# Optimization experiments

Measured on AMD Instinct MI355X. Metric: run time of the kernel, lower is better.

## Reference

```python
import jax, jax.numpy as jnp
import numpy as np

B, N, K, D, H = 8, 128, 64, 256, 8  # batch, groups, keys-per-query, k_dim (=h_size), n_head


def setup_inputs() -> dict:
    key = jax.random.key(0)
    kq, kk, kv, kw, kb = jax.random.split(key, 5)
    bound = 1.0 / np.sqrt(D)  # torch nn.Bilinear default init bound
    return {
        "q": jax.random.normal(kq, (B, N, 1, D), jnp.float32),
        "k": jax.random.normal(kk, (B, N, K, D), jnp.float32),
        "v": jax.random.normal(kv, (B, N, K, D), jnp.float32),
        "W": jax.random.uniform(kw, (H, D, D), jnp.float32, -bound, bound),
        "b": jax.random.uniform(kb, (H,), jnp.float32, -bound, bound),
    }


def reference(q, k, v, W, b):
    Bs, Ns, Ks, Ds = k.shape
    Hh = W.shape[0]
    qe = q[:, :, 0, :]  # (B,N,D); torch expands q over K, einsum broadcasts instead
    # nn.Bilinear: scores[b,n,k,h] = q[b,n,:] @ W[h] @ k[b,n,k,:] + b[h]
    scores = jnp.einsum('bnd,hde,bnke->bnkh', qe, W, k) + b  # (B,N,K,H)
    # Faithful to torch's .view(B, N, -1, K): row-major reinterpretation of the
    # trailing (K, H) pair as (H, K) — a dim-mixing reshape, not a transpose.
    attn = scores.reshape(Bs, Ns, Hh, Ks)
    attn = jax.nn.softmax(attn, axis=-1)  # softmax over last dim (dropout p=0)
    # matmul(attn, v) -> (B,N,H,Dv); then sum over the head axis
    output = jnp.einsum('bnhk,bnkd->bnd', attn, v)
    return output, attn
```

## Files before the change

kernel.cpp:

```cpp
#include <hip/hip_runtime.h>
#include <math.h>

namespace {

constexpr int D = 256;
constexpr int H = 8;

typedef __attribute__((ext_vector_type(8))) short bf16x8;
typedef __attribute__((ext_vector_type(4))) float f32x4;

__device__ inline unsigned short bf16rn(float x) {
  unsigned u = __builtin_bit_cast(unsigned, x);
  u += 0x7fffu + ((u >> 16) & 1u);
  return (unsigned short)(u >> 16);
}
__device__ inline float bf16tof(unsigned short b) {
  return __builtin_bit_cast(float, (unsigned)b << 16);
}

constexpr size_t OFF_QW  = 0;
constexpr size_t OFF_WFH = (size_t)8 << 20;
constexpr size_t OFF_WFL = (size_t)9 << 20;
constexpr size_t OFF_QFH = (size_t)10 << 20;
constexpr size_t OFF_QFL = ((size_t)10 << 20) + ((size_t)512 << 10);

__global__ __launch_bounds__(256) void prep_kernel(
    const float* __restrict__ q, const float* __restrict__ W,
    char* __restrict__ ws) {
  const int gid = blockIdx.x * 256 + threadIdx.x;
  float e[8];
  char *hi_base, *lo_base;
  size_t outoff;
  if (gid < 65536) {
    const int l = gid & 63, ks = (gid >> 6) & 7, he = gid >> 9;
    const int h = he >> 4, et = he & 15;
    const int d0 = ks * 32 + ((l >> 4) << 3);
    const int ecol = et * 16 + (l & 15);
    const float* src = W + (size_t)h * 65536 + (size_t)d0 * 256 + ecol;
    #pragma unroll
    for (int j = 0; j < 8; ++j) e[j] = src[j * 256];
    hi_base = ws + OFF_WFH; lo_base = ws + OFF_WFL;
    outoff = (size_t)gid * 16;
  } else {
    const int t = gid - 65536;
    const int l = t & 63, ks = (t >> 6) & 7, bt = t >> 9;
    const int row = bt * 16 + (l & 15);
    const int d0 = ks * 32 + ((l >> 4) << 3);
    const float4* src = reinterpret_cast<const float4*>(q + (size_t)row * 256 + d0);
    float4 a = src[0], b = src[1];
    e[0] = a.x; e[1] = a.y; e[2] = a.z; e[3] = a.w;
    e[4] = b.x; e[5] = b.y; e[6] = b.z; e[7] = b.w;
    hi_base = ws + OFF_QFH; lo_base = ws + OFF_QFL;
    outoff = (size_t)t * 16;
  }
  unsigned hw[4], lw[4];
  #pragma unroll
  for (int p = 0; p < 4; ++p) {
    unsigned short h0 = bf16rn(e[2 * p]), h1 = bf16rn(e[2 * p + 1]);
    unsigned short l0 = bf16rn(e[2 * p] - bf16tof(h0));
    unsigned short l1 = bf16rn(e[2 * p + 1] - bf16tof(h1));
    hw[p] = (unsigned)h0 | ((unsigned)h1 << 16);
    lw[p] = (unsigned)l0 | ((unsigned)l1 << 16);
  }
  *reinterpret_cast<uint4*>(hi_base + outoff) = make_uint4(hw[0], hw[1], hw[2], hw[3]);
  *reinterpret_cast<uint4*>(lo_base + outoff) = make_uint4(lw[0], lw[1], lw[2], lw[3]);
}

__global__ __launch_bounds__(256) void qw_mfma_kernel(
    const char* __restrict__ ws_in, float* __restrict__ qW) {
  const int tid = threadIdx.x;
  const int w   = blockIdx.x * 4 + (tid >> 6);
  const int l   = tid & 63;
  const int bng = w >> 5;
  const int heg = w & 31;
  const char* qfh = ws_in + OFF_QFH;
  const char* qfl = ws_in + OFF_QFL;
  const char* wfh = ws_in + OFF_WFH;
  const char* wfl = ws_in + OFF_WFL;

  f32x4 acc[2][4];
  #pragma unroll
  for (int i = 0; i < 2; ++i)
    #pragma unroll
    for (int j = 0; j < 4; ++j) acc[i][j] = {0.f, 0.f, 0.f, 0.f};

  #pragma unroll 2
  for (int ks = 0; ks < 8; ++ks) {
    bf16x8 aH[2], aL[2], bH[4], bL[4];
    #pragma unroll
    for (int i = 0; i < 2; ++i) {
      const size_t off = ((size_t)((bng * 2 + i) * 8 + ks) * 64 + l) * 16;
      aH[i] = *reinterpret_cast<const bf16x8*>(qfh + off);
      aL[i] = *reinterpret_cast<const bf16x8*>(qfl + off);
    }
    #pragma unroll
    for (int j = 0; j < 4; ++j) {
      const size_t off = ((size_t)((heg * 4 + j) * 8 + ks) * 64 + l) * 16;
      bH[j] = *reinterpret_cast<const bf16x8*>(wfh + off);
      bL[j] = *reinterpret_cast<const bf16x8*>(wfl + off);
    }
    #pragma unroll
    for (int i = 0; i < 2; ++i)
      #pragma unroll
      for (int j = 0; j < 4; ++j) {
        acc[i][j] = __builtin_amdgcn_mfma_f32_16x16x32_bf16(aH[i], bH[j], acc[i][j], 0, 0, 0);
        acc[i][j] = __builtin_amdgcn_mfma_f32_16x16x32_bf16(aH[i], bL[j], acc[i][j], 0, 0, 0);
        acc[i][j] = __builtin_amdgcn_mfma_f32_16x16x32_bf16(aL[i], bH[j], acc[i][j], 0, 0, 0);
      }
  }

  const int rbase = (l >> 4) * 4;
  const int col   = l & 15;
  #pragma unroll
  for (int i = 0; i < 2; ++i)
    #pragma unroll
    for (int j = 0; j < 4; ++j) {
      const size_t cidx = (size_t)(heg * 4 + j) * 16 + col;
      #pragma unroll
      for (int r = 0; r < 4; ++r) {
        const int bn = (bng * 2 + i) * 16 + rbase + r;
        qW[(size_t)bn * 2048 + cidx] = acc[i][j][r];
      }
    }
}

constexpr int FB2   = 0;
constexpr int WSP2  = 8320;
constexpr int SMEM3 = 9344;

__global__ __launch_bounds__(256, 2) void attn_fused_kernel(
    const float* __restrict__ qW, const float* __restrict__ kin,
    const float* __restrict__ vin, const float* __restrict__ bin,
    float* __restrict__ out, float* __restrict__ attn_out) {
  __shared__ alignas(16) long long smem_ll[SMEM3 / 8];
  char* sm = reinterpret_cast<char*>(smem_ll);
  float* wsp = reinterpret_cast<float*>(sm + WSP2);
  const int tid = threadIdx.x;
  const int bn  = blockIdx.x;
  const int wid = tid >> 6;
  const int ln  = tid & 63;

  const float* arow = kin + (size_t)bn * 16384 +
                      (size_t)(wid * 16 + (ln & 15)) * 256 + ((ln >> 4) << 3);
  float4 ka[16];
  #pragma unroll
  for (int ks = 0; ks < 8; ++ks) {
    ka[2 * ks]     = *reinterpret_cast<const float4*>(arow + ks * 32);
    ka[2 * ks + 1] = *reinterpret_cast<const float4*>(arow + ks * 32 + 4);
  }
  __builtin_amdgcn_sched_barrier(0);

  const float4* qw4 = reinterpret_cast<const float4*>(qW) + (size_t)bn * 512;
  float4 qv0 = qw4[tid];
  float4 qv1 = qw4[tid + 256];
  __builtin_amdgcn_sched_barrier(0);

  const float4* v4 = reinterpret_cast<const float4*>(vin) + (size_t)bn * 4096;
  float4 vv[16];
  #pragma unroll
  for (int i = 0; i < 16; ++i) vv[i] = v4[(size_t)(wid + 4 * i) * 64 + ln];
  __builtin_amdgcn_sched_barrier(0);

  {
    const int ks = tid >> 5, slot = 32 + (tid & 31);
    *reinterpret_cast<uint4*>(sm + FB2 + ks * 1040 + slot * 16) =
        make_uint4(0u, 0u, 0u, 0u);
  }
  #pragma unroll
  for (int i = 0; i < 2; ++i) {
    int p = tid + 256 * i;
    int hh = p >> 6, equad = p & 63;
    int ks = equad >> 3, g = (equad >> 1) & 3, j0 = (equad & 1) * 4;
    int base = FB2 + ks * 1040 + (hh * 4 + g) * 16 + j0 * 2;
    float4 qv = i == 0 ? qv0 : qv1;
    unsigned short h0 = bf16rn(qv.x), h1 = bf16rn(qv.y),
                   h2 = bf16rn(qv.z), h3 = bf16rn(qv.w);
    *reinterpret_cast<uint2*>(sm + base) =
        make_uint2((unsigned)h0 | ((unsigned)h1 << 16),
                   (unsigned)h2 | ((unsigned)h3 << 16));
  }
  __syncthreads();

  const int slot_r = (ln & 15) * 4 + (ln >> 4);
  const char* pbH = sm + FB2 + slot_r * 16;
  f32x4 acc = {0.f, 0.f, 0.f, 0.f};
  #pragma unroll
  for (int ks = 0; ks < 8; ++ks) {
    const float4 a0 = ka[2 * ks], a1 = ka[2 * ks + 1];
    bf16x8 aH;
    aH[0] = (short)bf16rn(a0.x); aH[1] = (short)bf16rn(a0.y);
    aH[2] = (short)bf16rn(a0.z); aH[3] = (short)bf16rn(a0.w);
    aH[4] = (short)bf16rn(a1.x); aH[5] = (short)bf16rn(a1.y);
    aH[6] = (short)bf16rn(a1.z); aH[7] = (short)bf16rn(a1.w);
    bf16x8 bH = *reinterpret_cast<const bf16x8*>(pbH + ks * 1040);
    acc = __builtin_amdgcn_mfma_f32_16x16x32_bf16(aH, bH, acc, 0, 0, 0);
  }

  const float bias = bin[ln & 7];
  const int col = ln & 15;
  const bool valid = col < 8;
  float x0 = acc[0] + bias, x1 = acc[1] + bias, x2 = acc[2] + bias, x3 = acc[3] + bias;
  float m = valid ? fmaxf(fmaxf(x0, x1), fmaxf(x2, x3)) : -1e30f;
  m = fmaxf(m, __shfl_xor(m, 1, 64));
  m = fmaxf(m, __shfl_xor(m, 2, 64));
  m = fmaxf(m, __shfl_xor(m, 4, 64));
  m = fmaxf(m, __shfl_xor(m, 16, 64));
  float e0 = valid ? expf(x0 - m) : 0.f;
  float e1 = valid ? expf(x1 - m) : 0.f;
  float e2 = valid ? expf(x2 - m) : 0.f;
  float e3 = valid ? expf(x3 - m) : 0.f;
  float s = e0 + e1 + e2 + e3;
  s += __shfl_xor(s, 1, 64);
  s += __shfl_xor(s, 2, 64);
  s += __shfl_xor(s, 4, 64);
  s += __shfl_xor(s, 16, 64);
  float inv = 1.f / s;
  float p0 = e0 * inv, p1 = e1 * inv, p2 = e2 * inv, p3 = e3 * inv;
  if (valid) {
    size_t base = (size_t)bn * 512 + (size_t)(wid * 16 + (ln >> 4) * 4) * 8 + col;
    attn_out[base]      = p0;
    attn_out[base + 8]  = p1;
    attn_out[base + 16] = p2;
    attn_out[base + 24] = p3;
  }
  p0 += __shfl_xor(p0, 32, 64);
  p1 += __shfl_xor(p1, 32, 64);
  p2 += __shfl_xor(p2, 32, 64);
  p3 += __shfl_xor(p3, 32, 64);
  if (ln < 32 && (ln & 15) < 8) {
    const int rb = (ln >> 4) * 4;
    const int c8 = ln & 7;
    float* w = wsp + wid * 64;
    w[(rb + 0) * 8 + c8] = p0;
    w[(rb + 1) * 8 + c8] = p1;
    w[(rb + 2) * 8 + c8] = p2;
    w[(rb + 3) * 8 + c8] = p3;
  }
  __syncthreads();

  float4 av = make_float4(0.f, 0.f, 0.f, 0.f);
  #pragma unroll
  for (int i = 0; i < 16; ++i) {
    const int r = wid + 4 * i;
    float w = wsp[r] + wsp[64 + r] + wsp[128 + r] + wsp[192 + r];
    av.x += w * vv[i].x; av.y += w * vv[i].y;
    av.z += w * vv[i].z; av.w += w * vv[i].w;
  }
  float* s_red = reinterpret_cast<float*>(sm);
  *reinterpret_cast<float4*>(&s_red[wid * 260 + (ln << 2)]) = av;
  __syncthreads();

  out[(size_t)bn * D + tid] =
      s_red[tid] + s_red[260 + tid] + s_red[520 + tid] + s_red[780 + tid];
}

}

extern "C" void kernel_launch(void* const* d_in, const int* in_sizes, int n_in,
                              void* d_out, int out_size, void* d_ws, size_t ws_size,
                              hipStream_t stream) {
  const float* q = (const float*)d_in[0];
  const float* k = (const float*)d_in[1];
  const float* v = (const float*)d_in[2];
  const float* W = (const float*)d_in[3];
  const float* b = (const float*)d_in[4];

  float* out  = (float*)d_out;
  float* attn = out + 262144;
  char*  ws   = (char*)d_ws;
  float* qWbuf = (float*)(ws + OFF_QW);

  hipLaunchKernelGGL(prep_kernel,       dim3(384),  dim3(256), 0, stream, q, W, ws);
  hipLaunchKernelGGL(qw_mfma_kernel,    dim3(256),  dim3(256), 0, stream, ws, qWbuf);
  hipLaunchKernelGGL(attn_fused_kernel, dim3(1024), dim3(256), 0, stream,
                     qWbuf, k, v, b, out, attn);
}
```

Before: 44.21 us.

## Split attention block into separate score and value-accumulate warp groups

Doubles the block to 512 threads. Waves 0-3 now load k and compute the bilinear scores and softmax, while waves 4-7 load v and do the weighted sum, so each wave holds only one 16-element register array instead of two. This is meant to lower per-wave register pressure and raise memory-level parallelism and occupancy. The cost is half the threads idling in each phase and more waves per block competing for the CU.

```diff
diff --git a/kernel.cpp b/kernel.cpp
--- a/kernel.cpp
+++ b/kernel.cpp
@@ -128,7 +128,7 @@
 constexpr int WSP2  = 8320;
 constexpr int SMEM3 = 9344;
 
-__global__ __launch_bounds__(256, 2) void attn_fused_kernel(
+__global__ __launch_bounds__(512, 8) void attn_fused_kernel(
     const float* __restrict__ qW, const float* __restrict__ kin,
     const float* __restrict__ vin, const float* __restrict__ bin,
     float* __restrict__ out, float* __restrict__ attn_out) {
@@ -139,40 +139,37 @@
   const int bn  = blockIdx.x;
   const int wid = tid >> 6;
   const int ln  = tid & 63;
-
-  const float* arow = kin + (size_t)bn * 16384 +
-                      (size_t)(wid * 16 + (ln & 15)) * 256 + ((ln >> 4) << 3);
+  const bool is_score = wid < 4;
+
   float4 ka[16];
-  #pragma unroll
-  for (int ks = 0; ks < 8; ++ks) {
-    ka[2 * ks]     = *reinterpret_cast<const float4*>(arow + ks * 32);
-    ka[2 * ks + 1] = *reinterpret_cast<const float4*>(arow + ks * 32 + 4);
-  }
-  __builtin_amdgcn_sched_barrier(0);
+  float4 vv[16];
+  if (is_score) {
+    const float* arow = kin + (size_t)bn * 16384 +
+                        (size_t)(wid * 16 + (ln & 15)) * 256 + ((ln >> 4) << 3);
+    #pragma unroll
+    for (int ks = 0; ks < 8; ++ks) {
+      ka[2 * ks]     = *reinterpret_cast<const float4*>(arow + ks * 32);
+      ka[2 * ks + 1] = *reinterpret_cast<const float4*>(arow + ks * 32 + 4);
+    }
+  } else {
+    const float4* v4 = reinterpret_cast<const float4*>(vin) + (size_t)bn * 4096;
+    #pragma unroll
+    for (int i = 0; i < 16; ++i)
+      vv[i] = v4[(size_t)((wid - 4) + 4 * i) * 64 + ln];
+  }
 
   const float4* qw4 = reinterpret_cast<const float4*>(qW) + (size_t)bn * 512;
-  float4 qv0 = qw4[tid];
-  float4 qv1 = qw4[tid + 256];
-  __builtin_amdgcn_sched_barrier(0);
-
-  const float4* v4 = reinterpret_cast<const float4*>(vin) + (size_t)bn * 4096;
-  float4 vv[16];
-  #pragma unroll
-  for (int i = 0; i < 16; ++i) vv[i] = v4[(size_t)(wid + 4 * i) * 64 + ln];
-  __builtin_amdgcn_sched_barrier(0);
-
-  {
+  float4 qv = qw4[tid];
+
+  if (tid < 256) {
     const int ks = tid >> 5, slot = 32 + (tid & 31);
     *reinterpret_cast<uint4*>(sm + FB2 + ks * 1040 + slot * 16) =
         make_uint4(0u, 0u, 0u, 0u);
   }
-  #pragma unroll
-  for (int i = 0; i < 2; ++i) {
-    int p = tid + 256 * i;
-    int hh = p >> 6, equad = p & 63;
-    int ks = equad >> 3, g = (equad >> 1) & 3, j0 = (equad & 1) * 4;
-    int base = FB2 + ks * 1040 + (hh * 4 + g) * 16 + j0 * 2;
-    float4 qv = i == 0 ? qv0 : qv1;
+  {
+    const int hh = tid >> 6, equad = tid & 63;
+    const int ks = equad >> 3, g = (equad >> 1) & 3, j0 = (equad & 1) * 4;
+    const int base = FB2 + ks * 1040 + (hh * 4 + g) * 16 + j0 * 2;
     unsigned short h0 = bf16rn(qv.x), h1 = bf16rn(qv.y),
                    h2 = bf16rn(qv.z), h3 = bf16rn(qv.w);
     *reinterpret_cast<uint2*>(sm + base) =
@@ -181,77 +178,83 @@
   }
   __syncthreads();
 
-  const int slot_r = (ln & 15) * 4 + (ln >> 4);
-  const char* pbH = sm + FB2 + slot_r * 16;
-  f32x4 acc = {0.f, 0.f, 0.f, 0.f};
-  #pragma unroll
-  for (int ks = 0; ks < 8; ++ks) {
-    const float4 a0 = ka[2 * ks], a1 = ka[2 * ks + 1];
-    bf16x8 aH;
-    aH[0] = (short)bf16rn(a0.x); aH[1] = (short)bf16rn(a0.y);
-    aH[2] = (short)bf16rn(a0.z); aH[3] = (short)bf16rn(a0.w);
-    aH[4] = (short)bf16rn(a1.x); aH[5] = (short)bf16rn(a1.y);
-    aH[6] = (short)bf16rn(a1.z); aH[7] = (short)bf16rn(a1.w);
-    bf16x8 bH = *reinterpret_cast<const bf16x8*>(pbH + ks * 1040);
-    acc = __builtin_amdgcn_mfma_f32_16x16x32_bf16(aH, bH, acc, 0, 0, 0);
-  }
-
-  const float bias = bin[ln & 7];
-  const int col = ln & 15;
-  const bool valid = col < 8;
-  float x0 = acc[0] + bias, x1 = acc[1] + bias, x2 = acc[2] + bias, x3 = acc[3] + bias;
-  float m = valid ? fmaxf(fmaxf(x0, x1), fmaxf(x2, x3)) : -1e30f;
-  m = fmaxf(m, __shfl_xor(m, 1, 64));
-  m = fmaxf(m, __shfl_xor(m, 2, 64));
-  m = fmaxf(m, __shfl_xor(m, 4, 64));
-  m = fmaxf(m, __shfl_xor(m, 16, 64));
-  float e0 = valid ? expf(x0 - m) : 0.f;
-  float e1 = valid ? expf(x1 - m) : 0.f;
-  float e2 = valid ? expf(x2 - m) : 0.f;
-  float e3 = valid ? expf(x3 - m) : 0.f;
-  float s = e0 + e1 + e2 + e3;
-  s += __shfl_xor(s, 1, 64);
-  s += __shfl_xor(s, 2, 64);
-  s += __shfl_xor(s, 4, 64);
-  s += __shfl_xor(s, 16, 64);
-  float inv = 1.f / s;
-  float p0 = e0 * inv, p1 = e1 * inv, p2 = e2 * inv, p3 = e3 * inv;
-  if (valid) {
-    size_t base = (size_t)bn * 512 + (size_t)(wid * 16 + (ln >> 4) * 4) * 8 + col;
-    attn_out[base]      = p0;
-    attn_out[base + 8]  = p1;
-    attn_out[base + 16] = p2;
-    attn_out[base + 24] = p3;
-  }
-  p0 += __shfl_xor(p0, 32, 64);
-  p1 += __shfl_xor(p1, 32, 64);
-  p2 += __shfl_xor(p2, 32, 64);
-  p3 += __shfl_xor(p3, 32, 64);
-  if (ln < 32 && (ln & 15) < 8) {
-    const int rb = (ln >> 4) * 4;
-    const int c8 = ln & 7;
-    float* w = wsp + wid * 64;
-    w[(rb + 0) * 8 + c8] = p0;
-    w[(rb + 1) * 8 + c8] = p1;
-    w[(rb + 2) * 8 + c8] = p2;
-    w[(rb + 3) * 8 + c8] = p3;
+  if (is_score) {
+    const int slot_r = (ln & 15) * 4 + (ln >> 4);
+    const char* pbH = sm + FB2 + slot_r * 16;
+    f32x4 acc = {0.f, 0.f, 0.f, 0.f};
+    #pragma unroll
+    for (int ks = 0; ks < 8; ++ks) {
+      const float4 a0 = ka[2 * ks], a1 = ka[2 * ks + 1];
+      bf16x8 aH;
+      aH[0] = (short)bf16rn(a0.x); aH[1] = (short)bf16rn(a0.y);
+      aH[2] = (short)bf16rn(a0.z); aH[3] = (short)bf16rn(a0.w);
+      aH[4] = (short)bf16rn(a1.x); aH[5] = (short)bf16rn(a1.y);
+      aH[6] = (short)bf16rn(a1.z); aH[7] = (short)bf16rn(a1.w);
+      bf16x8 bH = *reinterpret_cast<const bf16x8*>(pbH + ks * 1040);
+      acc = __builtin_amdgcn_mfma_f32_16x16x32_bf16(aH, bH, acc, 0, 0, 0);
+    }
+
+    const float bias = bin[ln & 7];
+    const int col = ln & 15;
+    const bool valid = col < 8;
+    float x0 = acc[0] + bias, x1 = acc[1] + bias, x2 = acc[2] + bias, x3 = acc[3] + bias;
+    float m = valid ? fmaxf(fmaxf(x0, x1), fmaxf(x2, x3)) : -1e30f;
+    m = fmaxf(m, __shfl_xor(m, 1, 64));
+    m = fmaxf(m, __shfl_xor(m, 2, 64));
+    m = fmaxf(m, __shfl_xor(m, 4, 64));
+    m = fmaxf(m, __shfl_xor(m, 16, 64));
+    float e0 = valid ? expf(x0 - m) : 0.f;
+    float e1 = valid ? expf(x1 - m) : 0.f;
+    float e2 = valid ? expf(x2 - m) : 0.f;
+    float e3 = valid ? expf(x3 - m) : 0.f;
+    float s = e0 + e1 + e2 + e3;
+    s += __shfl_xor(s, 1, 64);
+    s += __shfl_xor(s, 2, 64);
+    s += __shfl_xor(s, 4, 64);
+    s += __shfl_xor(s, 16, 64);
+    float inv = 1.f / s;
+    float p0 = e0 * inv, p1 = e1 * inv, p2 = e2 * inv, p3 = e3 * inv;
+    if (valid) {
+      size_t base = (size_t)bn * 512 + (size_t)(wid * 16 + (ln >> 4) * 4) * 8 + col;
+      attn_out[base]      = p0;
+      attn_out[base + 8]  = p1;
+      attn_out[base + 16] = p2;
+      attn_out[base + 24] = p3;
+    }
+    p0 += __shfl_xor(p0, 32, 64);
+    p1 += __shfl_xor(p1, 32, 64);
+    p2 += __shfl_xor(p2, 32, 64);
+    p3 += __shfl_xor(p3, 32, 64);
+    if (ln < 32 && (ln & 15) < 8) {
+      const int rb = (ln >> 4) * 4;
+      const int c8 = ln & 7;
+      float* w = wsp + wid * 64;
+      w[(rb + 0) * 8 + c8] = p0;
+      w[(rb + 1) * 8 + c8] = p1;
+      w[(rb + 2) * 8 + c8] = p2;
+      w[(rb + 3) * 8 + c8] = p3;
+    }
   }
   __syncthreads();
 
-  float4 av = make_float4(0.f, 0.f, 0.f, 0.f);
-  #pragma unroll
-  for (int i = 0; i < 16; ++i) {
-    const int r = wid + 4 * i;
-    float w = wsp[r] + wsp[64 + r] + wsp[128 + r] + wsp[192 + r];
-    av.x += w * vv[i].x; av.y += w * vv[i].y;
-    av.z += w * vv[i].z; av.w += w * vv[i].w;
-  }
   float* s_red = reinterpret_cast<float*>(sm);
-  *reinterpret_cast<float4*>(&s_red[wid * 260 + (ln << 2)]) = av;
+  if (!is_score) {
+    float4 av = make_float4(0.f, 0.f, 0.f, 0.f);
+    #pragma unroll
+    for (int i = 0; i < 16; ++i) {
+      const int r = (wid - 4) + 4 * i;
+      float w = wsp[r] + wsp[64 + r] + wsp[128 + r] + wsp[192 + r];
+      av.x += w * vv[i].x; av.y += w * vv[i].y;
+      av.z += w * vv[i].z; av.w += w * vv[i].w;
+    }
+    *reinterpret_cast<float4*>(&s_red[(wid - 4) * 260 + (ln << 2)]) = av;
+  }
   __syncthreads();
 
-  out[(size_t)bn * D + tid] =
-      s_red[tid] + s_red[260 + tid] + s_red[520 + tid] + s_red[780 + tid];
+  if (tid < 256) {
+    out[(size_t)bn * D + tid] =
+        s_red[tid] + s_red[260 + tid] + s_red[520 + tid] + s_red[780 + tid];
+  }
 }
 
 }
@@ -272,6 +275,6 @@
 
   hipLaunchKernelGGL(prep_kernel,       dim3(384),  dim3(256), 0, stream, q, W, ws);
   hipLaunchKernelGGL(qw_mfma_kernel,    dim3(256),  dim3(256), 0, stream, ws, qWbuf);
-  hipLaunchKernelGGL(attn_fused_kernel, dim3(1024), dim3(256), 0, stream,
+  hipLaunchKernelGGL(attn_fused_kernel, dim3(1024), dim3(512), 0, stream,
                      qWbuf, k, v, b, out, attn);
 }
```

Measured after the change: 121.7 us. 2.75x slower.
